# Kernel tuning notes

Hardware: AMD Instinct MI355X
Metric: run time of the kernel (lower is better)

Reference implementation:

```python
import math
import jax, jax.numpy as jnp
import numpy as np

BATCH, HEAD, LENGTH, D_K = 2, 8, 2048, 128
ROUNDS, N_BUCKETS = 4, 32
NEG_BIG, NEG_SMALL = -1e9, -1e5


def look_back(x):
    # x: [B, n_buckets/2, 2*bl, ...] -> [B, n_buckets/2, 4*bl, ...]
    # shift buckets by one (wrap-around) along bucket axis, concat on chunk axis
    return jnp.concatenate([jnp.roll(x, 1, axis=1), x], axis=2)


def setup_inputs() -> dict:
    key = jax.random.key(0)
    k1, k2, k3 = jax.random.split(key, 3)
    B = BATCH * HEAD
    return {
        "query": jax.random.normal(k1, (BATCH, HEAD, LENGTH, D_K), jnp.float32),
        "value": jax.random.normal(k2, (BATCH, HEAD, LENGTH, D_K), jnp.float32),
        "mask": jnp.ones((BATCH, LENGTH), dtype=bool),
        "rand_matrix": jax.random.normal(k3, (B, D_K, ROUNDS, N_BUCKETS // 2), jnp.float32),
        "seed": 0,
    }


def reference(query, value, mask, rand_matrix, seed):
    batch, head, L, D = query.shape
    B = batch * head
    R = ROUNDS
    nb2 = N_BUCKETS // 2
    bl = L // N_BUCKETS
    bl2, bl4 = 2 * bl, 4 * bl
    bi = jnp.arange(B)[:, None, None]  # batch index for fancy gathers

    # --- LSH hashing ---
    q = query / jnp.linalg.norm(query, axis=-1, keepdims=True)
    fq = q.reshape(B, L, D)
    rm = rand_matrix / jnp.linalg.norm(rand_matrix, axis=1, keepdims=True)
    h = jnp.einsum('bld,bdrk->blrk', fq, rm)          # [B,L,R,nb2]
    hashes = jnp.argmax(jnp.concatenate([h, -h], axis=-1), axis=-1)  # [B,L,R]

    # --- sort tokens by hash (per round) ---
    hash_indices = jnp.argsort(hashes, axis=1)                        # [B,L,R]
    sorted_hashes = jnp.take_along_axis(hashes, hash_indices, axis=1)
    original_indices = jnp.argsort(hash_indices, axis=1)              # inverse perm

    # --- reorder queries into buckets ---
    rq = fq[bi, hash_indices]                  # [B,L,R,D]
    rq = jnp.moveaxis(rq, 2, 3).reshape(B, nb2, bl2, D, R)
    lk = look_back(rq)                         # [B,nb2,bl4,D,R]
    scores = jnp.einsum('bnidr,bnjdr->bnijr', rq, lk) / math.sqrt(D)  # [B,nb2,bl2,bl4,R]

    # --- padding mask ---
    fm = jnp.broadcast_to(mask[:, None, :], (batch, head, L)).reshape(B, L)
    rmask = fm[bi, hash_indices].reshape(B, nb2, bl2, R)
    lb_mask = look_back(rmask)                 # [B,nb2,bl4,R]
    scores = jnp.where(lb_mask[:, :, None, :, :], scores, NEG_BIG)

    # --- same-hash mask ---
    sh = sorted_hashes.reshape(B, nb2, bl2, R)
    lh = look_back(sh)
    scores = jnp.where(sh[:, :, :, None, :] != lh[:, :, None, :, :], NEG_BIG, scores)

    # --- causal + self-attention masks ---
    qi = hash_indices.reshape(B, nb2, bl2, R)
    ki = look_back(qi)                         # [B,nb2,bl4,R]
    scores = jnp.where(qi[:, :, :, None, :] < ki[:, :, None, :, :], NEG_BIG, scores)
    scores = jnp.where(qi[:, :, :, None, :] == ki[:, :, None, :, :], NEG_SMALL, scores)

    # --- duplicate-key counting across rounds ---
    eki = jnp.broadcast_to(ki[:, :, None, :, :], (B, nb2, bl2, bl4, R)).reshape(B, L, bl4, R)
    oi_b = jnp.broadcast_to(original_indices[:, :, None, :], (B, L, bl4, R))
    rki = jnp.take_along_axis(eki, oi_b, axis=1)               # key ids per query, orig order
    flat = rki.reshape(B * L, bl4 * R).astype(jnp.int32)
    order = jnp.argsort(flat, axis=1)
    s = jnp.take_along_axis(flat, order, axis=1)
    counts = jnp.ones(s.shape, jnp.float32)
    for i in range(1, R):
        eq = (s[:, i:] == s[:, :-i]).astype(jnp.float32)
        counts = counts.at[:, i:].add(eq)
        counts = counts.at[:, :-i].add(eq)
    inv = jnp.argsort(order, axis=1)
    count_key = jnp.take_along_axis(counts, inv, axis=1).reshape(B, L, bl4, R)

    # --- softmax over all rounds (dedup-corrected) ---
    scores_flat = scores.reshape(B, L, bl4, R)
    scores_g = jnp.take_along_axis(scores_flat, oi_b, axis=1)
    scores_g = scores_g - jax.lax.stop_gradient(jnp.log(count_key))
    p = jax.nn.softmax(scores_g.reshape(B, L, bl4 * R), axis=-1).reshape(B, L, bl4, R)

    # --- value combine ---
    fv = value.reshape(B, L, D)
    rv = fv[bi, hash_indices]                  # [B,L,R,D]
    rv = jnp.moveaxis(rv, 2, 3).reshape(B, nb2, bl2, D, R)
    lv = look_back(rv)                         # [B,nb2,bl4,D,R]

    ai = jnp.broadcast_to(hash_indices[:, :, None, :], (B, L, bl4, R))
    rp = jnp.take_along_axis(p, ai, axis=1).reshape(B, nb2, bl2, bl4, R)
    att = jnp.einsum('bnijr,bnjdr->bnidr', rp, lv).reshape(B, L, D, R)
    oi_d = jnp.broadcast_to(original_indices[:, :, None, :], (B, L, D, R))
    att = jnp.take_along_axis(att, oi_d, axis=1).sum(axis=-1)  # sum over rounds
    return att.reshape(batch, head, L, D)
```

## Files before the change

kernel.cpp:

```cpp
#include <hip/hip_runtime.h>
#include <hip/hip_bf16.h>
#include <stdint.h>

constexpr int BH  = 16;
constexpr int LEN = 2048;
constexpr int DK  = 128;
constexpr int RND = 4;
constexpr int NB2 = 16;
constexpr int BL2 = 128;

typedef __attribute__((ext_vector_type(8)))  short short8;
typedef __attribute__((ext_vector_type(4)))  float f32x4;
typedef __attribute__((ext_vector_type(16))) float f32x16;

__device__ __forceinline__ float bflo(uint32_t u){ return __uint_as_float(u << 16); }
__device__ __forceinline__ uint16_t f2b(float x){
  uint32_t u = __float_as_uint(x);
  return (uint16_t)((u + 0x7fffu + ((u >> 16) & 1u)) >> 16);
}
__device__ __forceinline__ uint32_t pk2(float a, float b){
  return (uint32_t)f2b(a) | ((uint32_t)f2b(b) << 16);
}

__global__ __launch_bounds__(256) void k_hash(const float* __restrict__ q,
    const float* __restrict__ v, const float* __restrict__ rm,
    uint16_t* __restrict__ fqb, uint16_t* __restrict__ vbb,
    uint8_t* __restrict__ hsh)
{
  __shared__ float rm_s[128*64];
  __shared__ float qT[128*64];
  __shared__ float invn_s[64];
  int b = blockIdx.x >> 5, chunk = blockIdx.x & 31;
  int t = threadIdx.x;
  const float4* rm4 = (const float4*)(rm + (size_t)b*8192);
  #pragma unroll
  for (int i=0;i<8;i++) ((float4*)rm_s)[i*256 + t] = rm4[i*256 + t];
  int tl = t >> 2, qq = t & 3;
  int tok = chunk*64 + tl;
  size_t ro = ((size_t)b*LEN + tok)*DK;
  float qs[32];
  float ss = 0.f;
  #pragma unroll
  for (int i=0;i<8;i++){
    float4 w = *(const float4*)(q + ro + qq*32 + i*4);
    qs[i*4]=w.x; qs[i*4+1]=w.y; qs[i*4+2]=w.z; qs[i*4+3]=w.w;
    ss += w.x*w.x + w.y*w.y + w.z*w.z + w.w*w.w;
  }
  ss += __shfl_xor(ss,1); ss += __shfl_xor(ss,2);
  float rn = 1.0f / sqrtf(ss);
  #pragma unroll
  for (int i=0;i<32;i++) qs[i] *= rn;
  #pragma unroll
  for (int i=0;i<4;i++){
    uint4 u;
    u.x = pk2(qs[i*8+0], qs[i*8+1]); u.y = pk2(qs[i*8+2], qs[i*8+3]);
    u.z = pk2(qs[i*8+4], qs[i*8+5]); u.w = pk2(qs[i*8+6], qs[i*8+7]);
    *(uint4*)(fqb + ro + qq*32 + i*8) = u;
  }
  #pragma unroll
  for (int i=0;i<4;i++){
    float4 a = *(const float4*)(v + ro + qq*32 + i*8);
    float4 c = *(const float4*)(v + ro + qq*32 + i*8 + 4);
    uint4 u;
    u.x = pk2(a.x,a.y); u.y = pk2(a.z,a.w); u.z = pk2(c.x,c.y); u.w = pk2(c.z,c.w);
    *(uint4*)(vbb + ro + qq*32 + i*8) = u;
  }
  #pragma unroll
  for (int i=0;i<32;i++) qT[(qq*32+i)*64 + tl] = qs[i];
  __syncthreads();
  if (t < 64){
    float s2 = 0.f;
    for (int d=0; d<128; d++){ float w = rm_s[d*64+t]; s2 += w*w; }
    invn_s[t] = 1.0f / sqrtf(s2);
  }
  int tt = t & 15, cc = t >> 4;
  f32x4 a0={0,0,0,0}, a1={0,0,0,0}, a2={0,0,0,0}, a3={0,0,0,0};
  const float* qTp = qT   + tt*4;
  const float* rmp = rm_s + cc*4;
  #pragma unroll 8
  for (int d=0; d<128; d++){
    float4 qv = *(const float4*)(qTp + d*64);
    float4 rv = *(const float4*)(rmp + d*64);
    a0[0]+=qv.x*rv.x; a0[1]+=qv.x*rv.y; a0[2]+=qv.x*rv.z; a0[3]+=qv.x*rv.w;
    a1[0]+=qv.y*rv.x; a1[1]+=qv.y*rv.y; a1[2]+=qv.y*rv.z; a1[3]+=qv.y*rv.w;
    a2[0]+=qv.z*rv.x; a2[1]+=qv.z*rv.y; a2[2]+=qv.z*rv.z; a2[3]+=qv.z*rv.w;
    a3[0]+=qv.w*rv.x; a3[1]+=qv.w*rv.y; a3[2]+=qv.w*rv.z; a3[3]+=qv.w*rv.w;
  }
  __syncthreads();
  float rin[4];
  #pragma unroll
  for (int j=0;j<4;j++) rin[j] = invn_s[cc*4+j];
  int r = cc >> 2;
  int m = cc & 3;
  float bp[4], bn[4]; int bip[4], bin[4];
  #pragma unroll
  for (int i=0;i<4;i++){ bp[i]=-1e30f; bn[i]=-1e30f; bip[i]=0; bin[i]=16; }
  #pragma unroll
  for (int j=0;j<4;j++){
    int col = m*4 + j;
    #pragma unroll
    for (int i=0;i<4;i++){
      float hv = (i==0?a0[j]:i==1?a1[j]:i==2?a2[j]:a3[j]) * rin[j];
      if ( hv > bp[i]){ bp[i] =  hv; bip[i] = col; }
      if (-hv > bn[i]){ bn[i] = -hv; bin[i] = col + 16; }
    }
  }
  #pragma unroll
  for (int off=16; off<=32; off<<=1){
    #pragma unroll
    for (int i=0;i<4;i++){
      float op = __shfl_xor(bp[i], off); int oip = __shfl_xor(bip[i], off);
      if (op > bp[i] || (op == bp[i] && oip < bip[i])){ bp[i]=op; bip[i]=oip; }
      float on = __shfl_xor(bn[i], off); int oin = __shfl_xor(bin[i], off);
      if (on > bn[i] || (on == bn[i] && oin < bin[i])){ bn[i]=on; bin[i]=oin; }
    }
  }
  if (m == 0){
    uint32_t pk = 0;
    #pragma unroll
    for (int i=0;i<4;i++){
      int bidx = (bn[i] > bp[i]) ? bin[i] : bip[i];
      pk |= (uint32_t)bidx << (8*i);
    }
    *(uint32_t*)(hsh + ((size_t)(b*RND + r))*LEN + chunk*64 + tt*4) = pk;
  }
}

__global__ __launch_bounds__(256) void k_sort(const uint8_t* __restrict__ hsh,
    int* __restrict__ posA, int* __restrict__ tokA)
{
  __shared__ int hist[32*256];
  __shared__ int wtot[4];
  int br = blockIdx.x;
  int t = threadIdx.x;
  const uint8_t* hh = hsh + (size_t)br*LEN;
  uint8_t ub[8];
  #pragma unroll
  for (int i=0;i<8;i++) ub[i] = hh[t*8+i];
  #pragma unroll
  for (int k=0;k<32;k++) hist[k*256+t] = 0;
  __syncthreads();
  #pragma unroll
  for (int i=0;i<8;i++) hist[(int)ub[i]*256 + t] += 1;
  __syncthreads();
  int base = t*32, s0 = 0;
  for (int e=0;e<32;e++) s0 += hist[base+e];
  int x = s0;
  #pragma unroll
  for (int off=1; off<64; off<<=1){
    int y = __shfl_up(x, off);
    if ((t & 63) >= off) x += y;
  }
  if ((t & 63) == 63) wtot[t>>6] = x;
  __syncthreads();
  int add = 0;
  #pragma unroll
  for (int i2=0;i2<4;i2++) add += (i2 < (t>>6)) ? wtot[i2] : 0;
  int run = x - s0 + add;
  for (int e=0;e<32;e++){ int tmp = hist[base+e]; hist[base+e] = run; run += tmp; }
  __syncthreads();
  #pragma unroll
  for (int i=0;i<8;i++){
    int l = t*8+i, k = ub[i];
    int p = hist[k*256+t]++;
    posA[(size_t)br*LEN + l] = p;
    tokA[(size_t)br*LEN + p] = l | (k << 11);
  }
}

__global__ __launch_bounds__(256) void k_meta(
    const int* __restrict__ posA, const int* __restrict__ tokA, int* __restrict__ meta)
{
  int idx = blockIdx.x*256 + threadIdx.x;
  int br = idx >> 11;
  int b = br >> 2;
  int raw = tokA[idx];
  int tok = raw & 2047;
  int code = 0;
  #pragma unroll
  for (int r2=0;r2<4;r2++){
    int p = posA[(size_t)(b*4+r2)*LEN + tok];
    code |= (p >> 7) << (4*r2);
  }
  meta[idx] = raw | (code<<16);
}

__global__ __launch_bounds__(256, 3) void k_fattn(
    const uint16_t* __restrict__ fqb, const uint16_t* __restrict__ vbb,
    const int* __restrict__ meta, uint16_t* __restrict__ attb,
    float* __restrict__ rowsum)
{
  __shared__ __align__(16) char smem[39936];
  uint16_t* Ks  = (uint16_t*)smem;
  uint16_t* Vs2 = (uint16_t*)(smem + 8704);
  uint16_t* VT  = (uint16_t*)(smem + 17408);
  uint16_t* Ps  = (uint16_t*)(smem + 27648);
  uint2*    km2 = (uint2*)(smem + 37888);
  uint16_t* Qb  = (uint16_t*)smem;

  int bid = blockIdx.x;
  int n = bid & 15, r = (bid>>4)&3, b = bid>>6;
  int t = threadIdx.x;
  int w = t >> 6, lane = t & 63, l31 = lane & 31, h = lane >> 5;
  int br = b*RND + r;
  int sbase = br*LEN, qs0 = n*BL2;
  size_t gbase = (size_t)b*LEN;

  {
    int sk = (t < BL2) ? (((n+NB2-1)&15)*BL2 + t) : (n*BL2 + t - BL2);
    int km = meta[sbase + sk];
    uint32_t ck = ((uint32_t)km) >> 16;
    uint32_t ckp1 = ((ck & 0x7777u) + 0x1111u) ^ (ck & 0x8888u);
    uint2 kv; kv.x = (uint32_t)(km & 0xFFFF); kv.y = ck | (ckp1 << 16);
    km2[t] = kv;
  }
  int mq = meta[sbase + qs0 + w*32 + l31];
  uint32_t mq16 = (uint32_t)(mq & 0xFFFF);
  uint32_t cq = ((uint32_t)mq) >> 16;
  short8 qf[8];
  {
    const uint16_t* qrow = fqb + (gbase + (mq & 2047))*DK + h*8;
    #pragma unroll
    for (int dc=0;dc<8;dc++) qf[dc] = *(const short8*)(qrow + dc*16);
  }

  f32x16 O[4];
  #pragma unroll
  for (int i=0;i<4;i++)
    #pragma unroll
    for (int j=0;j<16;j++) O[i][j] = 0.f;
  float rsp = 0.f;

  int srow = t >> 3, sgp = t & 7;
  __syncthreads();
  {
    int tok = (int)(km2[srow].x & 2047u);
    const uint16_t* fr = fqb + (gbase + tok)*DK;
    const uint16_t* vr = vbb + (gbase + tok)*DK;
    #pragma unroll
    for (int i=0;i<2;i++){
      int ge = sgp*2 + i;
      *(uint4*)(Ks  + srow*136 + ge*8) = *(const uint4*)(fr + ge*8);
      *(uint4*)(Vs2 + srow*136 + ge*8) = *(const uint4*)(vr + ge*8);
    }
  }

  int d2 = t >> 1, kh = t & 1;

  for (int c=0;c<8;c++){
    __syncthreads();
    f32x16 S;
    #pragma unroll
    for (int j=0;j<16;j++) S[j] = 0.f;
    #pragma unroll
    for (int dc=0;dc<8;dc++){
      short8 a = *(const short8*)(Ks + l31*136 + dc*16 + h*8);
      S = __builtin_amdgcn_mfma_f32_32x32x16_bf16(a, qf[dc], S, 0, 0, 0);
    }
    {
      uint16_t tmp[16];
      #pragma unroll
      for (int jj=0;jj<16;jj++) tmp[jj] = Vs2[(kh*16 + jj)*136 + d2];
      *(uint4*)(VT + d2*40 + kh*16)     = *(uint4*)(tmp);
      *(uint4*)(VT + d2*40 + kh*16 + 8) = *(uint4*)(tmp + 8);
    }
    #pragma unroll
    for (int g=0; g<4; g++){
      const uint4* kp = (const uint4*)(km2 + c*32 + 8*g + 4*h);
      uint4 ka = kp[0], kb = kp[1];
      uint32_t kmv[4] = {ka.x, ka.z, kb.x, kb.z};
      uint32_t cky[4] = {ka.y, ka.w, kb.y, kb.w};
      uint32_t uu[4];
      #pragma unroll
      for (int rr=0; rr<4; rr++){
        uint32_t km16 = kmv[rr];
        uint32_t ck   = cky[rr] & 0xFFFFu;
        uint32_t ckp1 = cky[rr] >> 16;
        uint32_t xr = mq16 ^ km16;
        uint32_t x1 = cq ^ ck, x2 = cq ^ ckp1;
        uint32_t h1 = ~(((x1 & 0x7777u) + 0x7777u) | x1) & 0x8888u;
        uint32_t h2 = ~(((x2 & 0x7777u) + 0x7777u) | x2) & 0x8888u;
        uint32_t msum = (h1 >> 3) + (h2 >> 3);
        uint32_t cnt = ((msum * 0x1111u) >> 12) & 15u;
        float rcf = __builtin_amdgcn_rcpf((float)cnt);
        float Sv = S[g*4 + rr];
        float arg = fmaf(Sv, 0.12751743f, -0.14426950f);
        arg = (xr == 0u) ? -43.425121f : arg;
        bool kill = (xr >= 2048u) | (mq16 < km16);
        arg = kill ? -1e9f : arg;
        float e = __builtin_amdgcn_exp2f(arg) * rcf;
        rsp += e;
        uu[rr] = __float_as_uint(e);
      }
      uint2 pw;
      pw.x = __builtin_amdgcn_perm(uu[1], uu[0], 0x07060302);
      pw.y = __builtin_amdgcn_perm(uu[3], uu[2], 0x07060302);
      *(uint2*)(Ps + (w*32 + l31)*40 + 8*g + 4*h) = pw;
    }
    __syncthreads();
    if (c < 7){
      int tok = (int)(km2[(c+1)*32 + srow].x & 2047u);
      const uint16_t* fr = fqb + (gbase + tok)*DK;
      const uint16_t* vr = vbb + (gbase + tok)*DK;
      #pragma unroll
      for (int i=0;i<2;i++){
        int ge = sgp*2 + i;
        *(uint4*)(Ks  + srow*136 + ge*8) = *(const uint4*)(fr + ge*8);
        *(uint4*)(Vs2 + srow*136 + ge*8) = *(const uint4*)(vr + ge*8);
      }
    }
    short8 pb0 = *(const short8*)(Ps + (w*32 + l31)*40      + h*8);
    short8 pb1 = *(const short8*)(Ps + (w*32 + l31)*40 + 16 + h*8);
    #pragma unroll
    for (int dt=0; dt<4; dt++){
      short8 va0 = *(const short8*)(VT + (dt*32 + l31)*40      + h*8);
      short8 va1 = *(const short8*)(VT + (dt*32 + l31)*40 + 16 + h*8);
      O[dt] = __builtin_amdgcn_mfma_f32_32x32x16_bf16(va0, pb0, O[dt], 0, 0, 0);
      O[dt] = __builtin_amdgcn_mfma_f32_32x32x16_bf16(va1, pb1, O[dt], 0, 0, 0);
    }
  }
  rsp += __shfl_xor(rsp, 32);
  if (lane < 32) rowsum[sbase + qs0 + w*32 + l31] = rsp;
  #pragma unroll
  for (int p=0;p<2;p++){
    __syncthreads();
    if ((w>>1) == p){
      int qloc = (w&1)*32 + l31;
      #pragma unroll
      for (int dt=0; dt<4; dt++)
        #pragma unroll
        for (int g=0; g<4; g++){
          uint2 ow;
          ow.x = pk2(O[dt][g*4+0], O[dt][g*4+1]);
          ow.y = pk2(O[dt][g*4+2], O[dt][g*4+3]);
          *(uint2*)(Qb + qloc*136 + dt*32 + 8*g + 4*h) = ow;
        }
    }
    __syncthreads();
    #pragma unroll
    for (int i=0;i<4;i++){
      int ch = t + i*256;
      int row = ch >> 4, c16 = ch & 15;
      uint4 u = *(const uint4*)(Qb + row*136 + c16*8);
      *(uint4*)(attb + ((size_t)(sbase + qs0 + p*64 + row))*DK + c16*8) = u;
    }
  }
}

__global__ __launch_bounds__(256) void k_out(const uint16_t* __restrict__ attb,
    const float* __restrict__ rowsum, const int* __restrict__ posA,
    float* __restrict__ out)
{
  int idx = blockIdx.x*2 + (threadIdx.x >> 7);
  int tt = threadIdx.x & 127;
  int b = idx >> 11;
  int l = idx & (LEN-1);
  float num = 0.f, den = 0.f;
  #pragma unroll
  for (int r=0;r<4;r++){
    int sp = posA[(size_t)(b*RND+r)*LEN + l];
    size_t ro = ((size_t)(b*RND+r)*LEN + sp);
    num += bflo((uint32_t)attb[ro*DK + tt]);
    den += rowsum[ro];
  }
  out[(size_t)idx*DK + tt] = num / den;
}

extern "C" void kernel_launch(void* const* d_in, const int* in_sizes, int n_in,
                              void* d_out, int out_size, void* d_ws, size_t ws_size,
                              hipStream_t stream)
{
  const float* q  = (const float*)d_in[0];
  const float* v  = (const float*)d_in[1];
  const float* rm = (const float*)d_in[3];
  float* out = (float*)d_out;

  char* w = (char*)d_ws;
  uint16_t* fqb    = (uint16_t*)(w + 0);
  uint16_t* vbb    = (uint16_t*)(w + 8388608);
  uint8_t*  hsh    = (uint8_t*) (w + 16777216);
  int*      posA   = (int*)     (w + 16908288);
  int*      tokA   = (int*)     (w + 17432576);
  int*      meta   = (int*)     (w + 17956864);
  float*    rowsum = (float*)   (w + 18481152);
  uint16_t* attb   = (uint16_t*)(w + 19005440);

  k_hash <<<dim3(BH*32),          dim3(256), 0, stream>>>(q, v, rm, fqb, vbb, hsh);
  k_sort <<<dim3(BH*RND),         dim3(256), 0, stream>>>(hsh, posA, tokA);
  k_meta <<<dim3(BH*RND*LEN/256), dim3(256), 0, stream>>>(posA, tokA, meta);
  k_fattn<<<dim3(BH*RND*NB2),     dim3(256), 0, stream>>>(fqb, vbb, meta, attb, rowsum);
  k_out  <<<dim3(BH*LEN/2),       dim3(256), 0, stream>>>(attb, rowsum, posA, out);
}
```

Baseline: 166.0 us.

## Pass P through registers via permlane32 swap and pack key metadata as 16-bit pairs

The attention kernel no longer writes the probability tile to shared memory and reads it back. It builds the MFMA B-operand directly in registers using v_permlane32_swap, which removes the Ps buffer and shrinks LDS so more blocks can fit per CU. Key metadata is repacked as pairs of 16-bit values so two keys' dedup counts are computed with one SWAR pass, and tokens get a separate small array. It also remaps block indices to interleave blocks across batch/round, and pads the sort histogram to avoid LDS bank conflicts. The register-level lane swap relies on the exact MFMA lane layout, so a layout mismatch would give wrong results.

```diff
diff --git a/kernel.cpp b/kernel.cpp
--- a/kernel.cpp
+++ b/kernel.cpp
@@ -129,7 +129,7 @@
 __global__ __launch_bounds__(256) void k_sort(const uint8_t* __restrict__ hsh,
     int* __restrict__ posA, int* __restrict__ tokA)
 {
-  __shared__ int hist[32*256];
+  __shared__ int hist[32*257];
   __shared__ int wtot[4];
   int br = blockIdx.x;
   int t = threadIdx.x;
@@ -138,13 +138,13 @@
   #pragma unroll
   for (int i=0;i<8;i++) ub[i] = hh[t*8+i];
   #pragma unroll
-  for (int k=0;k<32;k++) hist[k*256+t] = 0;
-  __syncthreads();
-  #pragma unroll
-  for (int i=0;i<8;i++) hist[(int)ub[i]*256 + t] += 1;
-  __syncthreads();
-  int base = t*32, s0 = 0;
-  for (int e=0;e<32;e++) s0 += hist[base+e];
+  for (int k=0;k<32;k++) hist[k*257+t] = 0;
+  __syncthreads();
+  #pragma unroll
+  for (int i=0;i<8;i++) hist[(int)ub[i]*257 + t] += 1;
+  __syncthreads();
+  int base = (t>>3)*257 + (t&7)*32, s0 = 0;
+  for (int e=0;e<32;e++) s0 += hist[base + ((e + t) & 31)];
   int x = s0;
   #pragma unroll
   for (int off=1; off<64; off<<=1){
@@ -162,7 +162,7 @@
   #pragma unroll
   for (int i=0;i<8;i++){
     int l = t*8+i, k = ub[i];
-    int p = hist[k*256+t]++;
+    int p = hist[k*257+t]++;
     posA[(size_t)br*LEN + l] = p;
     tokA[(size_t)br*LEN + p] = l | (k << 11);
   }
@@ -190,15 +190,16 @@
     const int* __restrict__ meta, uint16_t* __restrict__ attb,
     float* __restrict__ rowsum)
 {
-  __shared__ __align__(16) char smem[39936];
+  __shared__ __align__(16) char smem[30208];
   uint16_t* Ks  = (uint16_t*)smem;
   uint16_t* Vs2 = (uint16_t*)(smem + 8704);
   uint16_t* VT  = (uint16_t*)(smem + 17408);
-  uint16_t* Ps  = (uint16_t*)(smem + 27648);
-  uint2*    km2 = (uint2*)(smem + 37888);
+  uint32_t* km4 = (uint32_t*)(smem + 27648);
+  uint16_t* tokS= (uint16_t*)(smem + 29696);
   uint16_t* Qb  = (uint16_t*)smem;
 
-  int bid = blockIdx.x;
+  int bid0 = blockIdx.x;
+  int bid = ((bid0 & 7) << 7) | (bid0 >> 3);
   int n = bid & 15, r = (bid>>4)&3, b = bid>>6;
   int t = threadIdx.x;
   int w = t >> 6, lane = t & 63, l31 = lane & 31, h = lane >> 5;
@@ -206,17 +207,29 @@
   int sbase = br*LEN, qs0 = n*BL2;
   size_t gbase = (size_t)b*LEN;
 
-  {
-    int sk = (t < BL2) ? (((n+NB2-1)&15)*BL2 + t) : (n*BL2 + t - BL2);
-    int km = meta[sbase + sk];
-    uint32_t ck = ((uint32_t)km) >> 16;
-    uint32_t ckp1 = ((ck & 0x7777u) + 0x1111u) ^ (ck & 0x8888u);
-    uint2 kv; kv.x = (uint32_t)(km & 0xFFFF); kv.y = ck | (ckp1 << 16);
-    km2[t] = kv;
+  if (t < 64){
+    uint32_t km[4], ck[4], cp[4];
+    #pragma unroll
+    for (int j=0;j<4;j++){
+      int sk4 = t*4 + j;
+      int sk = (sk4 < BL2) ? (((n+NB2-1)&15)*BL2 + sk4) : (n*BL2 + sk4 - BL2);
+      int kmw = meta[sbase + sk];
+      uint32_t ckv = ((uint32_t)kmw) >> 16;
+      km[j] = (uint32_t)kmw & 0xFFFFu;
+      ck[j] = ckv;
+      cp[j] = ((ckv & 0x7777u) + 0x1111u) ^ (ckv & 0x8888u);
+      tokS[sk4] = (uint16_t)(km[j] & 2047u);
+    }
+    uint32_t* gp = km4 + t*8;
+    gp[0] = km[0] | (km[1]<<16); gp[1] = km[2] | (km[3]<<16);
+    gp[2] = ck[0] | (ck[1]<<16); gp[3] = ck[2] | (ck[3]<<16);
+    gp[4] = cp[0] | (cp[1]<<16); gp[5] = cp[2] | (cp[3]<<16);
   }
   int mq = meta[sbase + qs0 + w*32 + l31];
   uint32_t mq16 = (uint32_t)(mq & 0xFFFF);
   uint32_t cq = ((uint32_t)mq) >> 16;
+  uint32_t mq2 = mq16 | (mq16 << 16);
+  uint32_t cq2 = cq | (cq << 16);
   short8 qf[8];
   {
     const uint16_t* qrow = fqb + (gbase + (mq & 2047))*DK + h*8;
@@ -234,7 +247,7 @@
   int srow = t >> 3, sgp = t & 7;
   __syncthreads();
   {
-    int tok = (int)(km2[srow].x & 2047u);
+    int tok = (int)tokS[srow];
     const uint16_t* fr = fqb + (gbase + tok)*DK;
     const uint16_t* vr = vbb + (gbase + tok)*DK;
     #pragma unroll
@@ -264,42 +277,52 @@
       *(uint4*)(VT + d2*40 + kh*16)     = *(uint4*)(tmp);
       *(uint4*)(VT + d2*40 + kh*16 + 8) = *(uint4*)(tmp + 8);
     }
+    uint32_t u[8];
     #pragma unroll
     for (int g=0; g<4; g++){
-      const uint4* kp = (const uint4*)(km2 + c*32 + 8*g + 4*h);
-      uint4 ka = kp[0], kb = kp[1];
-      uint32_t kmv[4] = {ka.x, ka.z, kb.x, kb.z};
-      uint32_t cky[4] = {ka.y, ka.w, kb.y, kb.w};
-      uint32_t uu[4];
+      const uint32_t* gp = km4 + (c*8 + 2*g + h)*8;
+      uint4 A  = *(const uint4*)gp;
+      uint2 Bv = *(const uint2*)(gp + 4);
       #pragma unroll
-      for (int rr=0; rr<4; rr++){
-        uint32_t km16 = kmv[rr];
-        uint32_t ck   = cky[rr] & 0xFFFFu;
-        uint32_t ckp1 = cky[rr] >> 16;
-        uint32_t xr = mq16 ^ km16;
-        uint32_t x1 = cq ^ ck, x2 = cq ^ ckp1;
-        uint32_t h1 = ~(((x1 & 0x7777u) + 0x7777u) | x1) & 0x8888u;
-        uint32_t h2 = ~(((x2 & 0x7777u) + 0x7777u) | x2) & 0x8888u;
-        uint32_t msum = (h1 >> 3) + (h2 >> 3);
-        uint32_t cnt = ((msum * 0x1111u) >> 12) & 15u;
-        float rcf = __builtin_amdgcn_rcpf((float)cnt);
-        float Sv = S[g*4 + rr];
-        float arg = fmaf(Sv, 0.12751743f, -0.14426950f);
-        arg = (xr == 0u) ? -43.425121f : arg;
-        bool kill = (xr >= 2048u) | (mq16 < km16);
-        arg = kill ? -1e9f : arg;
-        float e = __builtin_amdgcn_exp2f(arg) * rcf;
-        rsp += e;
-        uu[rr] = __float_as_uint(e);
+      for (int p=0; p<2; p++){
+        uint32_t kmp = p ? A.y : A.x;
+        uint32_t ckp = p ? A.w : A.z;
+        uint32_t cpp = p ? Bv.y : Bv.x;
+        uint32_t xr2 = mq2 ^ kmp;
+        uint32_t x1 = cq2 ^ ckp, x2 = cq2 ^ cpp;
+        uint32_t h1 = ~(((x1 & 0x77777777u) + 0x77777777u) | x1) & 0x88888888u;
+        uint32_t h2 = ~(((x2 & 0x77777777u) + 0x77777777u) | x2) & 0x88888888u;
+        uint32_t prod = ((h1 >> 3) + (h2 >> 3)) * 0x1111u;
+        uint32_t xr0 = xr2 & 0xFFFFu, xr1 = xr2 >> 16;
+        float rc0 = __builtin_amdgcn_rcpf((float)((prod >> 12) & 15u));
+        float rc1 = __builtin_amdgcn_rcpf((float)(prod >> 28));
+        float Sv0 = S[g*4 + 2*p], Sv1 = S[g*4 + 2*p + 1];
+        float a0 = fmaf(Sv0, 0.12751743f, -0.14426950f);
+        float a1 = fmaf(Sv1, 0.12751743f, -0.14426950f);
+        a0 = (xr0 == 0u) ? -43.425121f : a0;
+        a1 = (xr1 == 0u) ? -43.425121f : a1;
+        bool k0 = (xr0 >= 2048u) | (mq16 < (kmp & 0xFFFFu));
+        bool k1 = (xr1 >= 2048u) | (mq16 < (kmp >> 16));
+        a0 = k0 ? -1e9f : a0;
+        a1 = k1 ? -1e9f : a1;
+        float e0 = __builtin_amdgcn_exp2f(a0) * rc0;
+        float e1 = __builtin_amdgcn_exp2f(a1) * rc1;
+        rsp += e0 + e1;
+        u[g*2+p] = __builtin_amdgcn_perm(__float_as_uint(e1), __float_as_uint(e0),
+                                         0x07060302);
       }
-      uint2 pw;
-      pw.x = __builtin_amdgcn_perm(uu[1], uu[0], 0x07060302);
-      pw.y = __builtin_amdgcn_perm(uu[3], uu[2], 0x07060302);
-      *(uint2*)(Ps + (w*32 + l31)*40 + 8*g + 4*h) = pw;
-    }
+    }
+    asm volatile("v_permlane32_swap_b32 %0, %1" : "+v"(u[0]), "+v"(u[2]));
+    asm volatile("v_permlane32_swap_b32 %0, %1" : "+v"(u[1]), "+v"(u[3]));
+    asm volatile("v_permlane32_swap_b32 %0, %1" : "+v"(u[4]), "+v"(u[6]));
+    asm volatile("v_permlane32_swap_b32 %0, %1" : "+v"(u[5]), "+v"(u[7]));
+    union { uint32_t wu[4]; short8 v8; } pf0, pf1;
+    pf0.wu[0]=u[0]; pf0.wu[1]=u[1]; pf0.wu[2]=u[2]; pf0.wu[3]=u[3];
+    pf1.wu[0]=u[4]; pf1.wu[1]=u[5]; pf1.wu[2]=u[6]; pf1.wu[3]=u[7];
+    short8 pb0 = pf0.v8, pb1 = pf1.v8;
     __syncthreads();
     if (c < 7){
-      int tok = (int)(km2[(c+1)*32 + srow].x & 2047u);
+      int tok = (int)tokS[(c+1)*32 + srow];
       const uint16_t* fr = fqb + (gbase + tok)*DK;
       const uint16_t* vr = vbb + (gbase + tok)*DK;
       #pragma unroll
@@ -309,8 +332,6 @@
         *(uint4*)(Vs2 + srow*136 + ge*8) = *(const uint4*)(vr + ge*8);
       }
     }
-    short8 pb0 = *(const short8*)(Ps + (w*32 + l31)*40      + h*8);
-    short8 pb1 = *(const short8*)(Ps + (w*32 + l31)*40 + 16 + h*8);
     #pragma unroll
     for (int dt=0; dt<4; dt++){
       short8 va0 = *(const short8*)(VT + (dt*32 + l31)*40      + h*8);
@@ -341,8 +362,8 @@
     for (int i=0;i<4;i++){
       int ch = t + i*256;
       int row = ch >> 4, c16 = ch & 15;
-      uint4 u = *(const uint4*)(Qb + row*136 + c16*8);
-      *(uint4*)(attb + ((size_t)(sbase + qs0 + p*64 + row))*DK + c16*8) = u;
+      uint4 u2 = *(const uint4*)(Qb + row*136 + c16*8);
+      *(uint4*)(attb + ((size_t)(sbase + qs0 + p*64 + row))*DK + c16*8) = u2;
     }
   }
 }
```

After: 157.9 us. -4.9%, faster.
